# Kernel optimization log

Hardware: AMD Instinct MI355X
Metric: run time of the kernel (lower is better)

Reference implementation:

```python
import jax, jax.numpy as jnp
import numpy as np

N_EMBED = 384
NUM_EXPERTS = 8
TOP_K = 2


def setup_inputs() -> dict:
    key = jax.random.key(0)
    k_x, k_n, k_w1, k_b1, k_w2, k_b2 = jax.random.split(key, 6)
    B, T = 16, 4096
    bound = 1.0 / np.sqrt(N_EMBED)
    return {
        "x": jax.random.normal(k_x, (B, T, N_EMBED), dtype=jnp.float32),
        "noise": jax.random.normal(k_n, (B, T, NUM_EXPERTS), dtype=jnp.float32),
        "w_route": jax.random.uniform(k_w1, (NUM_EXPERTS, N_EMBED), jnp.float32, -bound, bound),
        "b_route": jax.random.uniform(k_b1, (NUM_EXPERTS,), jnp.float32, -bound, bound),
        "w_noise": jax.random.uniform(k_w2, (NUM_EXPERTS, N_EMBED), jnp.float32, -bound, bound),
        "b_noise": jax.random.uniform(k_b2, (NUM_EXPERTS,), jnp.float32, -bound, bound),
    }


def reference(x, noise, w_route, b_route, w_noise, b_noise):
    # two tiny linears: [B,T,D] @ [D,E] -> [B,T,E]
    logits = jnp.einsum("btd,ed->bte", x, w_route) + b_route
    noise_logits = jnp.einsum("btd,ed->bte", x, w_noise) + b_noise
    noisy_logits = logits + noise * jax.nn.softplus(noise_logits)

    top_k_logits, indices = jax.lax.top_k(noisy_logits, TOP_K)  # [B,T,k]

    # scatter top-k values into a -inf tensor; equivalently mask non-topk to -inf
    # (values at the top-k positions are exactly the noisy logits there)
    mask = jax.nn.one_hot(indices, NUM_EXPERTS, dtype=jnp.bool_).any(axis=-2)  # [B,T,E]
    sparse_logits = jnp.where(mask, noisy_logits, -jnp.inf)
    router_output = jax.nn.softmax(sparse_logits, axis=-1)
    return router_output, indices
```

## Files before the change

kernel.cpp:

```cpp
#include <hip/hip_runtime.h>
#include <math.h>


constexpr int D = 384;

__device__ __forceinline__ float dpp_xor1(float v) {
    return __int_as_float(__builtin_amdgcn_update_dpp(
        0, __float_as_int(v), 0xB1, 0xF, 0xF, true));
}
__device__ __forceinline__ float dpp_xor2(float v) {
    return __int_as_float(__builtin_amdgcn_update_dpp(
        0, __float_as_int(v), 0x4E, 0xF, 0xF, true));
}
__device__ __forceinline__ float swz_xor4(float v) {
    return __int_as_float(__builtin_amdgcn_ds_swizzle(__float_as_int(v), 0x101F));
}

__global__ __launch_bounds__(256, 4) void noisy_topk_router_f32(
    const float* __restrict__ x,
    const float* __restrict__ noise,
    const float* __restrict__ w_route,
    const float* __restrict__ b_route,
    const float* __restrict__ w_noise,
    const float* __restrict__ b_noise,
    float* __restrict__ out,
    int ntok)
{
    __shared__ float w_lds[16 * D];
    __shared__ float bias[16];

    const int tid = threadIdx.x;

#pragma unroll
    for (int r = 0; r < 3; ++r) {
        int i = (tid + 256 * r) * 4;
        *(float4*)(w_lds + i)        = *(const float4*)(w_route + i);
        *(float4*)(w_lds + 3072 + i) = *(const float4*)(w_noise + i);
    }
    if (tid < 8)       bias[tid] = b_route[tid];
    else if (tid < 16) bias[tid] = b_noise[tid - 8];
    __syncthreads();

    const int wave = tid >> 6;
    const int lane = tid & 63;
    const int tg   = lane >> 3;
    const int c    = lane & 7;
    const int token = blockIdx.x * 32 + wave * 8 + tg;

    float acc[16];
#pragma unroll
    for (int e = 0; e < 16; ++e) acc[e] = 0.f;

    const float* xr = x + (size_t)token * D + c * 4;

    float4 xa[3], xb[3];
#pragma unroll
    for (int qq = 0; qq < 3; ++qq)
        xa[qq] = *(const float4*)(xr + qq * 32);

#pragma unroll
    for (int s = 0; s < 4; ++s) {
        const int qn = (s < 3) ? (s + 1) * 3 : 0;
#pragma unroll
        for (int qq = 0; qq < 3; ++qq)
            xb[qq] = *(const float4*)(xr + (qn + qq) * 32);
#pragma unroll
        for (int qq = 0; qq < 3; ++qq) {
            const int q = s * 3 + qq;
            const float* wj = w_lds + q * 32 + c * 4;
#pragma unroll
            for (int e = 0; e < 16; ++e) {
                float4 wv = *(const float4*)(wj + e * D);
                acc[e] += xa[qq].x * wv.x + xa[qq].y * wv.y
                        + xa[qq].z * wv.z + xa[qq].w * wv.w;
            }
        }
#pragma unroll
        for (int qq = 0; qq < 3; ++qq) xa[qq] = xb[qq];
    }

#pragma unroll
    for (int e = 0; e < 16; ++e) acc[e] += dpp_xor1(acc[e]);
#pragma unroll
    for (int e = 0; e < 16; ++e) acc[e] += dpp_xor2(acc[e]);
#pragma unroll
    for (int e = 0; e < 16; ++e) acc[e] += swz_xor4(acc[e]);

    if (c == 0) {
        float4 n0 = *(const float4*)(noise + (size_t)token * 8);
        float4 n1 = *(const float4*)(noise + (size_t)token * 8 + 4);
        float nz[8] = {n0.x, n0.y, n0.z, n0.w, n1.x, n1.y, n1.z, n1.w};

        float noisy[8];
#pragma unroll
        for (int e = 0; e < 8; ++e) {
            float lg = acc[e] + bias[e];
            float nl = acc[8 + e] + bias[8 + e];
            float sp = fmaxf(nl, 0.f) + log1pf(expf(-fabsf(nl)));
            noisy[e] = lg + nz[e] * sp;
        }

        float v0 = noisy[0]; int i0 = 0;
#pragma unroll
        for (int e = 1; e < 8; ++e)
            if (noisy[e] > v0) { v0 = noisy[e]; i0 = e; }
        float v1 = -INFINITY; int i1 = 0;
#pragma unroll
        for (int e = 0; e < 8; ++e)
            if (e != i0 && noisy[e] > v1) { v1 = noisy[e]; i1 = e; }

        float ex  = expf(v1 - v0);
        float inv = 1.f / (1.f + ex);
        float p0  = inv;
        float p1  = ex * inv;

        float pr[8];
#pragma unroll
        for (int e = 0; e < 8; ++e)
            pr[e] = (e == i0) ? p0 : ((e == i1) ? p1 : 0.f);

        float* orow = out + (size_t)token * 8;
        *(float4*)(orow)     = make_float4(pr[0], pr[1], pr[2], pr[3]);
        *(float4*)(orow + 4) = make_float4(pr[4], pr[5], pr[6], pr[7]);

        *(float2*)(out + (size_t)ntok * 8 + (size_t)token * 2) =
            make_float2((float)i0, (float)i1);
    }
}

extern "C" void kernel_launch(void* const* d_in, const int* in_sizes, int n_in,
                              void* d_out, int out_size, void* d_ws, size_t ws_size,
                              hipStream_t stream) {
    const float* x       = (const float*)d_in[0];
    const float* noise   = (const float*)d_in[1];
    const float* w_route = (const float*)d_in[2];
    const float* b_route = (const float*)d_in[3];
    const float* w_noise = (const float*)d_in[4];
    const float* b_noise = (const float*)d_in[5];
    float* out = (float*)d_out;

    const int ntok   = in_sizes[0] / D;
    const int blocks = ntok / 32;

    hipLaunchKernelGGL(noisy_topk_router_f32, dim3(blocks), dim3(256), 0, stream,
                       x, noise, w_route, b_route, w_noise, b_noise, out, ntok);
}
```

Baseline: 169.9 us.

## Read router weights from global/L1 instead of LDS; nontemporal x loads

Removes the per-block LDS staging of both weight matrices and the block barrier, and has each lane read weight float4s directly from global memory, relying on L1/L2 caching. Streaming x loads use nontemporal hints so they do not evict the weights. Biases are loaded directly in the epilogue, the redundant prefetch in the last stage is dropped, and launch bounds ask for higher occupancy. The risk is that per-lane weight reads now go through the vector cache, which may have lower bandwidth than LDS.

```diff
diff --git a/kernel.cpp b/kernel.cpp
--- a/kernel.cpp
+++ b/kernel.cpp
@@ -3,6 +3,13 @@
 
 
 constexpr int D = 384;
+
+typedef float vfloat4 __attribute__((ext_vector_type(4)));
+
+__device__ __forceinline__ float4 ntload4(const float* p) {
+    vfloat4 v = __builtin_nontemporal_load((const vfloat4*)p);
+    return make_float4(v.x, v.y, v.z, v.w);
+}
 
 __device__ __forceinline__ float dpp_xor1(float v) {
     return __int_as_float(__builtin_amdgcn_update_dpp(
@@ -16,7 +23,7 @@
     return __int_as_float(__builtin_amdgcn_ds_swizzle(__float_as_int(v), 0x101F));
 }
 
-__global__ __launch_bounds__(256, 4) void noisy_topk_router_f32(
+__global__ __launch_bounds__(256, 8) void noisy_topk_router_f32(
     const float* __restrict__ x,
     const float* __restrict__ noise,
     const float* __restrict__ w_route,
@@ -26,21 +33,7 @@
     float* __restrict__ out,
     int ntok)
 {
-    __shared__ float w_lds[16 * D];
-    __shared__ float bias[16];
-
-    const int tid = threadIdx.x;
-
-#pragma unroll
-    for (int r = 0; r < 3; ++r) {
-        int i = (tid + 256 * r) * 4;
-        *(float4*)(w_lds + i)        = *(const float4*)(w_route + i);
-        *(float4*)(w_lds + 3072 + i) = *(const float4*)(w_noise + i);
-    }
-    if (tid < 8)       bias[tid] = b_route[tid];
-    else if (tid < 16) bias[tid] = b_noise[tid - 8];
-    __syncthreads();
-
+    const int tid  = threadIdx.x;
     const int wave = tid >> 6;
     const int lane = tid & 63;
     const int tg   = lane >> 3;
@@ -51,32 +44,43 @@
 #pragma unroll
     for (int e = 0; e < 16; ++e) acc[e] = 0.f;
 
-    const float* xr = x + (size_t)token * D + c * 4;
+    const float* xr  = x + (size_t)token * D + c * 4;
+    const float* wre = w_route + c * 4;
+    const float* wno = w_noise + c * 4;
 
     float4 xa[3], xb[3];
 #pragma unroll
     for (int qq = 0; qq < 3; ++qq)
-        xa[qq] = *(const float4*)(xr + qq * 32);
+        xa[qq] = ntload4(xr + qq * 32);
 
 #pragma unroll
     for (int s = 0; s < 4; ++s) {
-        const int qn = (s < 3) ? (s + 1) * 3 : 0;
+        if (s < 3) {
+            const int qn = (s + 1) * 3;
 #pragma unroll
-        for (int qq = 0; qq < 3; ++qq)
-            xb[qq] = *(const float4*)(xr + (qn + qq) * 32);
+            for (int qq = 0; qq < 3; ++qq)
+                xb[qq] = ntload4(xr + (qn + qq) * 32);
+        }
 #pragma unroll
         for (int qq = 0; qq < 3; ++qq) {
             const int q = s * 3 + qq;
-            const float* wj = w_lds + q * 32 + c * 4;
 #pragma unroll
-            for (int e = 0; e < 16; ++e) {
-                float4 wv = *(const float4*)(wj + e * D);
+            for (int e = 0; e < 8; ++e) {
+                float4 wv = *(const float4*)(wre + e * D + q * 32);
                 acc[e] += xa[qq].x * wv.x + xa[qq].y * wv.y
                         + xa[qq].z * wv.z + xa[qq].w * wv.w;
             }
+#pragma unroll
+            for (int e = 0; e < 8; ++e) {
+                float4 wv = *(const float4*)(wno + e * D + q * 32);
+                acc[8 + e] += xa[qq].x * wv.x + xa[qq].y * wv.y
+                            + xa[qq].z * wv.z + xa[qq].w * wv.w;
+            }
         }
+        if (s < 3) {
 #pragma unroll
-        for (int qq = 0; qq < 3; ++qq) xa[qq] = xb[qq];
+            for (int qq = 0; qq < 3; ++qq) xa[qq] = xb[qq];
+        }
     }
 
 #pragma unroll
@@ -91,11 +95,18 @@
         float4 n1 = *(const float4*)(noise + (size_t)token * 8 + 4);
         float nz[8] = {n0.x, n0.y, n0.z, n0.w, n1.x, n1.y, n1.z, n1.w};
 
+        float4 br0 = *(const float4*)(b_route);
+        float4 br1 = *(const float4*)(b_route + 4);
+        float4 bn0 = *(const float4*)(b_noise);
+        float4 bn1 = *(const float4*)(b_noise + 4);
+        float brr[8] = {br0.x, br0.y, br0.z, br0.w, br1.x, br1.y, br1.z, br1.w};
+        float bnn[8] = {bn0.x, bn0.y, bn0.z, bn0.w, bn1.x, bn1.y, bn1.z, bn1.w};
+
         float noisy[8];
 #pragma unroll
         for (int e = 0; e < 8; ++e) {
-            float lg = acc[e] + bias[e];
-            float nl = acc[8 + e] + bias[8 + e];
+            float lg = acc[e] + brr[e];
+            float nl = acc[8 + e] + bnn[e];
             float sp = fmaxf(nl, 0.f) + log1pf(expf(-fabsf(nl)));
             noisy[e] = lg + nz[e] * sp;
         }
```

Result: slower. 232.0 us (+36.5%).
